# Kernel optimization log

Measured on AMD Instinct MI355X. Metric: run time of the kernel, lower is better.

The kernel has to match this reference:

```python
import jax, jax.numpy as jnp
import numpy as np

D_MODEL = 1024
NUM_HEADS = 16
HEAD_DIM = D_MODEL // NUM_HEADS


def setup_inputs() -> dict:
    key = jax.random.key(0)
    kx, kq, kk, kv, ko = jax.random.split(key, 5)
    B, S = 2, 2048
    scale = 1.0 / np.sqrt(D_MODEL)
    return {
        "x": jax.random.normal(kx, (B, S, D_MODEL), dtype=jnp.float32),
        "W_q": jax.random.normal(kq, (D_MODEL, D_MODEL), dtype=jnp.float32) * scale,
        "W_k": jax.random.normal(kk, (D_MODEL, D_MODEL), dtype=jnp.float32) * scale,
        "W_v": jax.random.normal(kv, (D_MODEL, D_MODEL), dtype=jnp.float32) * scale,
        "W_o": jax.random.normal(ko, (D_MODEL, D_MODEL), dtype=jnp.float32) * scale,
        "causal": 1,
    }


def _attn(x, W_q, W_k, W_v, W_o, causal):
    B, S, D = x.shape
    H, Hd = NUM_HEADS, HEAD_DIM
    # projections: nn.Linear applies x @ W.T
    q = (x @ W_q.T).reshape(B, S, H, Hd)
    k = (x @ W_k.T).reshape(B, S, H, Hd)
    v = (x @ W_v.T).reshape(B, S, H, Hd)
    # scores: [B, H, S, S]
    scores = jnp.einsum("bqhd,bkhd->bhqk", q, k) / np.sqrt(Hd)
    if causal:
        mask = jnp.triu(jnp.ones((S, S), dtype=bool), k=1)
        scores = jnp.where(mask, -jnp.inf, scores)
    attn = jax.nn.softmax(scores, axis=-1)
    out = jnp.einsum("bhqk,bkhd->bqhd", attn, v).reshape(B, S, D)
    return out @ W_o.T


def reference(x, W_q, W_k, W_v, W_o, causal):
    return _attn(x, W_q, W_k, W_v, W_o, causal)
```

## Files before the change

kernel.cpp:

```cpp
#include <hip/hip_runtime.h>

typedef __attribute__((ext_vector_type(8))) short bf16x8;
typedef __attribute__((ext_vector_type(4))) float f32x4;
typedef __attribute__((ext_vector_type(4))) unsigned short u16x4;

#define MFMA16(a, b, c) __builtin_amdgcn_mfma_f32_16x16x32_bf16((a), (b), (c), 0, 0, 0)

static constexpr int D_MODEL = 1024;
static constexpr int SEQ = 2048;
static constexpr int NH = 16;
static constexpr int HD = 64;
static constexpr int LDA = 40;
static constexpr int MST = 136;
static constexpr float NEG_BIG = -1.0e30f;

__device__ __forceinline__ unsigned short f2bf(float f) {
  union { float f; unsigned int u; } v; v.f = f;
  unsigned int r = v.u + 0x7fffu + ((v.u >> 16) & 1u);
  return (unsigned short)(r >> 16);
}

__device__ __forceinline__ unsigned int cvtpk_bf16(float a, float b) {
  unsigned int r;
  asm("v_cvt_pk_bf16_f32 %0, %1, %2" : "=v"(r) : "v"(a), "v"(b));
  return r;
}

__device__ __forceinline__ bf16x8 ld8(const void* p, size_t eidx, int bf) {
  if (bf) return *(const bf16x8*)((const unsigned short*)p + eidx);
  const float* f = (const float*)p + eidx;
  f32x4 lo = *(const f32x4*)f;
  f32x4 hi = *(const f32x4*)(f + 4);
  bf16x8 r;
  r[0] = (short)f2bf(lo[0]); r[1] = (short)f2bf(lo[1]);
  r[2] = (short)f2bf(lo[2]); r[3] = (short)f2bf(lo[3]);
  r[4] = (short)f2bf(hi[0]); r[5] = (short)f2bf(hi[1]);
  r[6] = (short)f2bf(hi[2]); r[7] = (short)f2bf(hi[3]);
  return r;
}

__device__ __forceinline__ void async16(const unsigned short* g, unsigned short* l) {
  __builtin_amdgcn_global_load_lds(
      (const __attribute__((address_space(1))) void*)g,
      (__attribute__((address_space(3))) void*)l, 16, 0, 0);
}

__global__ __launch_bounds__(64) void detect_kernel(
    const unsigned short* __restrict__ xs, int* __restrict__ flag) {
  int lane = threadIdx.x;
  unsigned short s = xs[2 * lane];
  int e = (s >> 7) & 0xFF;
  bool hit = (e >= 117 && e <= 129);
  unsigned long long m = __ballot(hit);
  if (lane == 0) { flag[0] = (__popcll(m) >= 32) ? 1 : 0; flag[1] = 1; }
}

__global__ __launch_bounds__(256) void convert_kernel(
    const void* __restrict__ X,
    const void* __restrict__ W0, const void* __restrict__ W1,
    const void* __restrict__ W2, const void* __restrict__ W3,
    const int* __restrict__ flag,
    unsigned short* __restrict__ Xb, unsigned short* __restrict__ Wb)
{
  const int bf = *flag;
  const int ty = blockIdx.y;
  const void* src; unsigned short* dst; size_t n;
  if (ty == 0) { src = X; dst = Xb; n = (size_t)2 * SEQ * D_MODEL; }
  else {
    src = (ty == 1) ? W0 : (ty == 2) ? W1 : (ty == 3) ? W2 : W3;
    dst = Wb + (size_t)(ty - 1) * D_MODEL * D_MODEL;
    n = (size_t)D_MODEL * D_MODEL;
  }
  size_t i = ((size_t)blockIdx.x * 256 + threadIdx.x) * 8;
  if (i >= n) return;
  *(bf16x8*)(dst + i) = ld8(src, i, bf);
}

__device__ __forceinline__ void gemm_fast_core(
    const unsigned short* __restrict__ A, const unsigned short* __restrict__ B,
    int tm, int tn, unsigned short* smem, f32x4 acc[4][4])
{
  const int t = threadIdx.x;
  const int lane = t & 63;
  const int w = t >> 6;
  const int wm = (w >> 1) * 64, wn = (w & 1) * 64;
  const int quad = lane >> 4, l16 = lane & 15;
  const int srow = lane >> 3;
  const int scol = ((lane & 7) ^ srow) * 8;
  const int xa = l16 & 7;

#pragma unroll
  for (int mi = 0; mi < 4; ++mi)
#pragma unroll
    for (int ni = 0; ni < 4; ++ni)
      acc[mi][ni] = (f32x4){0.f, 0.f, 0.f, 0.f};

#pragma unroll
  for (int j = 0; j < 4; ++j) {
    const int row = w * 32 + j * 8;
    async16(A + (size_t)(tm + row + srow) * D_MODEL + scol, smem + row * 64);
    async16(B + (size_t)(tn + row + srow) * D_MODEL + scol,
            smem + 8192 + row * 64);
  }

  for (int kt = 0; kt < 16; ++kt) {
    const int co = (kt & 1) << 14;
    asm volatile("s_waitcnt vmcnt(0)" ::: "memory");
    __syncthreads();
    if (kt < 15) {
      const int no = ((kt & 1) ^ 1) << 14;
      const int k0 = (kt + 1) * 64;
#pragma unroll
      for (int j = 0; j < 4; ++j) {
        const int row = w * 32 + j * 8;
        async16(A + (size_t)(tm + row + srow) * D_MODEL + k0 + scol,
                smem + no + row * 64);
        async16(B + (size_t)(tn + row + srow) * D_MODEL + k0 + scol,
                smem + no + 8192 + row * 64);
      }
    }
    bf16x8 af[2][4], bfv[2][4];
#pragma unroll
    for (int ks = 0; ks < 2; ++ks) {
#pragma unroll
      for (int mi = 0; mi < 4; ++mi)
        af[ks][mi] = *(const bf16x8*)(smem + co + (wm + mi * 16 + l16) * 64 +
                                      ((ks * 4 + quad) ^ xa) * 8);
#pragma unroll
      for (int ni = 0; ni < 4; ++ni)
        bfv[ks][ni] = *(const bf16x8*)(smem + co + 8192 +
                                       (wn + ni * 16 + l16) * 64 +
                                       ((ks * 4 + quad) ^ xa) * 8);
    }
    __builtin_amdgcn_s_setprio(1);
#pragma unroll
    for (int ks = 0; ks < 2; ++ks)
#pragma unroll
      for (int mi = 0; mi < 4; ++mi)
#pragma unroll
        for (int ni = 0; ni < 4; ++ni)
          acc[mi][ni] = MFMA16(af[ks][mi], bfv[ks][ni], acc[mi][ni]);
    __builtin_amdgcn_s_setprio(0);
  }
}

__global__ __launch_bounds__(256) void qkv_fast_kernel(
    const unsigned short* __restrict__ X,
    const unsigned short* __restrict__ Wb,
    unsigned short* __restrict__ qd,
    unsigned short* __restrict__ kws,
    unsigned short* __restrict__ vws)
{
  __shared__ __align__(16) unsigned short smem[4 * 128 * 64];
  const int bid = blockIdx.x;
  const int xcd = bid & 7, s0 = bid >> 3;
  const int tmg = xcd >> 2, tng = xcd & 3;
  const int tm_local = s0 / 6, zt = s0 % 6;
  const int z = zt >> 1, tn_local = zt & 1;
  const int tm = (tmg * 16 + tm_local) * 128;
  const int tn = (tng * 2 + tn_local) * 128;
  const unsigned short* W = Wb + (size_t)z * D_MODEL * D_MODEL;
  f32x4 acc[4][4];
  gemm_fast_core(X, W, tm, tn, smem, acc);

  const int t = threadIdx.x;
  const int lane = t & 63, w = t >> 6;
  const int wm = (w >> 1) * 64, wn = (w & 1) * 64;
  const int quad = lane >> 4, l16 = lane & 15;

  if (z == 2) {
    const int b = tm >> 11;
    const int sb = tm & 2047;
#pragma unroll
    for (int ph = 0; ph < 2; ++ph) {
      __syncthreads();
      if ((w & 1) == ph) {
#pragma unroll
        for (int mi = 0; mi < 4; ++mi)
#pragma unroll
          for (int ni = 0; ni < 4; ++ni)
#pragma unroll
            for (int r = 0; r < 4; ++r) {
              int m_local = wm + mi * 16 + quad * 4 + r;
              int n_sub = ni * 16 + l16;
              smem[n_sub * MST + m_local] = f2bf(acc[mi][ni][r]);
            }
      }
      __syncthreads();
      const int row = t >> 2, c0 = (t & 3) * 32;
      const int n_g = tn + ph * 64 + row;
      const int h = n_g >> 6, d = n_g & 63;
      unsigned short* dst = vws + (((size_t)b * NH + h) * HD + d) * SEQ + sb + c0;
#pragma unroll
      for (int cc = 0; cc < 4; ++cc)
        *(bf16x8*)(dst + cc * 8) = *(const bf16x8*)(smem + row * MST + c0 + cc * 8);
    }
    return;
  }
#pragma unroll
  for (int mi = 0; mi < 4; ++mi)
#pragma unroll
    for (int ni = 0; ni < 4; ++ni)
#pragma unroll
      for (int r = 0; r < 4; ++r) {
        int m = tm + wm + mi * 16 + quad * 4 + r;
        int n = tn + wn + ni * 16 + l16;
        unsigned short bv = f2bf(acc[mi][ni][r]);
        if (z == 0) {
          qd[(size_t)m * D_MODEL + n] = bv;
        } else {
          int b = m >> 11, sg = m & 2047;
          int h = n >> 6, d = n & 63;
          kws[(((size_t)b * NH + h) * SEQ + sg) * HD + d] = bv;
        }
      }
}

__global__ __launch_bounds__(256) void oproj_fast_kernel(
    const unsigned short* __restrict__ AW,
    const unsigned short* __restrict__ Wo,
    float* __restrict__ tmp)
{
  __shared__ __align__(16) unsigned short smem[4 * 128 * 64];
  const int bid = blockIdx.x;
  const int xcd = bid & 7, s0 = bid >> 3;
  const int tmg = xcd >> 2, tng = xcd & 3;
  const int tm = (tmg * 16 + (s0 >> 1)) * 128;
  const int tn = (tng * 2 + (s0 & 1)) * 128;
  f32x4 acc[4][4];
  gemm_fast_core(AW, Wo, tm, tn, smem, acc);

  const int t = threadIdx.x;
  const int lane = t & 63, w = t >> 6;
  const int wm = (w >> 1) * 64, wn = (w & 1) * 64;
  const int quad = lane >> 4, l16 = lane & 15;
#pragma unroll
  for (int mi = 0; mi < 4; ++mi)
#pragma unroll
    for (int ni = 0; ni < 4; ++ni)
#pragma unroll
      for (int r = 0; r < 4; ++r) {
        int m = tm + wm + mi * 16 + quad * 4 + r;
        int n = tn + wn + ni * 16 + l16;
        tmp[(size_t)m * D_MODEL + n] = acc[mi][ni][r];
      }
}

__device__ __forceinline__ void gemm_tile_128x128(
    const void* __restrict__ A, const void* __restrict__ B, int bf,
    int tm, int tn, unsigned short* As, unsigned short* Bs, f32x4 acc[4][4])
{
  const int t = threadIdx.x;
  const int lane = t & 63;
  const int w = t >> 6;
  const int wm = (w >> 1) * 64, wn = (w & 1) * 64;
  const int quad = lane >> 4, l16 = lane & 15;
  const int r0 = t >> 2, kc = (t & 3) * 8;
  const int r1 = r0 + 64;

#pragma unroll
  for (int mi = 0; mi < 4; ++mi)
#pragma unroll
    for (int ni = 0; ni < 4; ++ni)
      acc[mi][ni] = (f32x4){0.f, 0.f, 0.f, 0.f};

  for (int k0 = 0; k0 < D_MODEL; k0 += 32) {
    bf16x8 a0 = ld8(A, (size_t)(tm + r0) * D_MODEL + k0 + kc, bf);
    bf16x8 a1 = ld8(A, (size_t)(tm + r1) * D_MODEL + k0 + kc, bf);
    bf16x8 b0 = ld8(B, (size_t)(tn + r0) * D_MODEL + k0 + kc, bf);
    bf16x8 b1 = ld8(B, (size_t)(tn + r1) * D_MODEL + k0 + kc, bf);
    __syncthreads();
    *(bf16x8*)(As + r0 * LDA + kc) = a0;
    *(bf16x8*)(As + r1 * LDA + kc) = a1;
    *(bf16x8*)(Bs + r0 * LDA + kc) = b0;
    *(bf16x8*)(Bs + r1 * LDA + kc) = b1;
    __syncthreads();
    bf16x8 af[4], bfv[4];
#pragma unroll
    for (int mi = 0; mi < 4; ++mi)
      af[mi] = *(const bf16x8*)(As + (wm + mi * 16 + l16) * LDA + quad * 8);
#pragma unroll
    for (int ni = 0; ni < 4; ++ni)
      bfv[ni] = *(const bf16x8*)(Bs + (wn + ni * 16 + l16) * LDA + quad * 8);
#pragma unroll
    for (int mi = 0; mi < 4; ++mi)
#pragma unroll
      for (int ni = 0; ni < 4; ++ni)
        acc[mi][ni] = MFMA16(af[mi], bfv[ni], acc[mi][ni]);
  }
}

__global__ __launch_bounds__(256) void qkv_kernel(
    const void* __restrict__ X,
    const void* __restrict__ Wq,
    const void* __restrict__ Wk,
    const void* __restrict__ Wv,
    const int* __restrict__ flag,
    unsigned short* __restrict__ qd,
    unsigned short* __restrict__ kws,
    unsigned short* __restrict__ vws)
{
  __shared__ __align__(16) unsigned short As[128 * LDA];
  __shared__ __align__(16) unsigned short Bs[128 * LDA];
  const int bf = *flag;
  const int z = blockIdx.z;
  const void* W = (z == 0) ? Wq : ((z == 1) ? Wk : Wv);
  const int tm = blockIdx.y * 128, tn = blockIdx.x * 128;
  f32x4 acc[4][4];
  gemm_tile_128x128(X, W, bf, tm, tn, As, Bs, acc);

  const int t = threadIdx.x;
  const int lane = t & 63, w = t >> 6;
  const int wm = (w >> 1) * 64, wn = (w & 1) * 64;
  const int quad = lane >> 4, l16 = lane & 15;
#pragma unroll
  for (int mi = 0; mi < 4; ++mi)
#pragma unroll
    for (int ni = 0; ni < 4; ++ni)
#pragma unroll
      for (int r = 0; r < 4; ++r) {
        int m = tm + wm + mi * 16 + quad * 4 + r;
        int n = tn + wn + ni * 16 + l16;
        unsigned short bv = f2bf(acc[mi][ni][r]);
        if (z == 0) {
          qd[(size_t)m * D_MODEL + n] = bv;
        } else {
          int b = m >> 11, s = m & 2047;
          int h = n >> 6, d = n & 63;
          if (z == 1) kws[(((size_t)b * NH + h) * SEQ + s) * HD + d] = bv;
          else        vws[(((size_t)b * NH + h) * HD + d) * SEQ + s] = bv;
        }
      }
}

__global__ __launch_bounds__(256) void oproj_kernel(
    const unsigned short* __restrict__ AW,
    const void* __restrict__ Wo,
    const int* __restrict__ flag,
    float* __restrict__ tmp)
{
  __shared__ __align__(16) unsigned short As[128 * LDA];
  __shared__ __align__(16) unsigned short Bs[128 * LDA];
  const int bf = *flag;
  const int t = threadIdx.x;
  const int lane = t & 63;
  const int w = t >> 6;
  const int wm = (w >> 1) * 64, wn = (w & 1) * 64;
  const int quad = lane >> 4, l16 = lane & 15;
  const int r0 = t >> 2, kc = (t & 3) * 8;
  const int r1 = r0 + 64;
  const int tm = blockIdx.y * 128, tn = blockIdx.x * 128;
  f32x4 acc[4][4];
#pragma unroll
  for (int mi = 0; mi < 4; ++mi)
#pragma unroll
    for (int ni = 0; ni < 4; ++ni)
      acc[mi][ni] = (f32x4){0.f, 0.f, 0.f, 0.f};

  for (int k0 = 0; k0 < D_MODEL; k0 += 32) {
    bf16x8 a0 = *(const bf16x8*)(AW + (size_t)(tm + r0) * D_MODEL + k0 + kc);
    bf16x8 a1 = *(const bf16x8*)(AW + (size_t)(tm + r1) * D_MODEL + k0 + kc);
    bf16x8 b0 = ld8(Wo, (size_t)(tn + r0) * D_MODEL + k0 + kc, bf);
    bf16x8 b1 = ld8(Wo, (size_t)(tn + r1) * D_MODEL + k0 + kc, bf);
    __syncthreads();
    *(bf16x8*)(As + r0 * LDA + kc) = a0;
    *(bf16x8*)(As + r1 * LDA + kc) = a1;
    *(bf16x8*)(Bs + r0 * LDA + kc) = b0;
    *(bf16x8*)(Bs + r1 * LDA + kc) = b1;
    __syncthreads();
    bf16x8 af[4], bfv[4];
#pragma unroll
    for (int mi = 0; mi < 4; ++mi)
      af[mi] = *(const bf16x8*)(As + (wm + mi * 16 + l16) * LDA + quad * 8);
#pragma unroll
    for (int ni = 0; ni < 4; ++ni)
      bfv[ni] = *(const bf16x8*)(Bs + (wn + ni * 16 + l16) * LDA + quad * 8);
#pragma unroll
    for (int mi = 0; mi < 4; ++mi)
#pragma unroll
      for (int ni = 0; ni < 4; ++ni)
        acc[mi][ni] = MFMA16(af[mi], bfv[ni], acc[mi][ni]);
  }
#pragma unroll
  for (int mi = 0; mi < 4; ++mi)
#pragma unroll
    for (int ni = 0; ni < 4; ++ni)
#pragma unroll
      for (int r = 0; r < 4; ++r) {
        int m = tm + wm + mi * 16 + quad * 4 + r;
        int n = tn + wn + ni * 16 + l16;
        tmp[(size_t)m * D_MODEL + n] = acc[mi][ni][r];
      }
}

__device__ __forceinline__ void attn_item(
    const unsigned short* __restrict__ Ksb, const unsigned short* __restrict__ Vsb,
    const bf16x8 (&aq)[2][2], f32x4 (&oaccT)[2][4], float (&lsum)[2],
    int kt, int diag, int q0base, int l16, int quad, int xa, float Cs)
{
  bf16x8 kfr[4][2], vfr[4][2];
#pragma unroll
  for (int cb = 0; cb < 4; ++cb)
#pragma unroll
    for (int hf = 0; hf < 2; ++hf) {
      kfr[cb][hf] = *(const bf16x8*)(Ksb + (cb * 16 + l16) * 64 +
                                     ((hf * 4 + quad) ^ xa) * 8);
      vfr[cb][hf] = *(const bf16x8*)(Vsb + (cb * 16 + l16) * 64 +
                                     ((hf * 4 + quad) ^ xa) * 8);
    }
#pragma unroll
  for (int s = 0; s < 2; ++s) {
    f32x4 sc[4];
    __builtin_amdgcn_s_setprio(1);
#pragma unroll
    for (int cb = 0; cb < 4; ++cb) {
      sc[cb] = (f32x4){0.f, 0.f, 0.f, 0.f};
      sc[cb] = MFMA16(kfr[cb][0], aq[s][0], sc[cb]);
      sc[cb] = MFMA16(kfr[cb][1], aq[s][1], sc[cb]);
    }
    __builtin_amdgcn_s_setprio(0);
    if (diag) {
      int qq = q0base + s * 16 + l16;
#pragma unroll
      for (int cb = 0; cb < 4; ++cb)
#pragma unroll
        for (int rr = 0; rr < 4; ++rr)
          if (kt * 64 + (cb & 1) * 32 + quad * 8 + (cb >> 1) * 4 + rr > qq)
            sc[cb][rr] = NEG_BIG;
    }
    float ls = 0.f;
#pragma unroll
    for (int cb = 0; cb < 4; ++cb)
#pragma unroll
      for (int rr = 0; rr < 4; ++rr) {
        float pv = __builtin_amdgcn_exp2f(sc[cb][rr] * Cs);
        ls += pv;
        sc[cb][rr] = pv;
      }
    lsum[s] += ls;
    bf16x8 bp[2];
#pragma unroll
    for (int hf = 0; hf < 2; ++hf) {
      union { unsigned int w4[4]; bf16x8 v; } u;
      u.w4[0] = cvtpk_bf16(sc[hf][0], sc[hf][1]);
      u.w4[1] = cvtpk_bf16(sc[hf][2], sc[hf][3]);
      u.w4[2] = cvtpk_bf16(sc[2 + hf][0], sc[2 + hf][1]);
      u.w4[3] = cvtpk_bf16(sc[2 + hf][2], sc[2 + hf][3]);
      bp[hf] = u.v;
    }
    __builtin_amdgcn_s_setprio(1);
#pragma unroll
    for (int db = 0; db < 4; ++db) {
      oaccT[s][db] = MFMA16(vfr[db][0], bp[0], oaccT[s][db]);
      oaccT[s][db] = MFMA16(vfr[db][1], bp[1], oaccT[s][db]);
    }
    __builtin_amdgcn_s_setprio(0);
  }
}

__global__ __launch_bounds__(128, 1) void attn_kernel(
    unsigned short* __restrict__ Qd,
    const unsigned short* __restrict__ Kb,
    const unsigned short* __restrict__ Vt,
    const int* __restrict__ causal_p)
{
  __shared__ __align__(16) unsigned short Ks[3][64 * 64];
  __shared__ __align__(16) unsigned short Vs[3][64 * 64];
  const int bid = blockIdx.x;
  const int xcd = bid & 7, slot = bid >> 3;
  const int bhl = slot >> 4, p = slot & 15;
  const int bh = xcd * 4 + bhl;
  const int b = bh >> 4, h = bh & 15;
  const int t = threadIdx.x, lane = t & 63, w = t >> 6;
  const int quad = lane >> 4, l16 = lane & 15;
  const int causal = *causal_p;
  const int tA = causal ? (31 - p) : (2 * p);
  const int tB = causal ? p : (2 * p + 1);
  const int ktA = causal ? (32 - p) : 32;
  const int ITEMS = causal ? 33 : 64;
  unsigned short* qh = Qd + (size_t)b * SEQ * D_MODEL + h * HD;
  const unsigned short* kh = Kb + ((size_t)b * NH + h) * SEQ * HD;
  const unsigned short* vh = Vt + ((size_t)b * NH + h) * HD * SEQ;
  const float Cs = 0.125f * 1.4426950408889634f;
  const int srow = lane >> 3;
  const int gcol = ((lane & 7) ^ srow) * 8;
  const int xa = l16 & 7;

  int kvp[4];
#pragma unroll
  for (int j2 = 0; j2 < 4; ++j2) {
    const int rp = w * 32 + j2 * 8 + srow;
    kvp[j2] = ((rp >> 4) & 1) * 32 + ((rp >> 2) & 3) * 8 + ((rp >> 5) & 1) * 4 + (rp & 3);
  }

  const int qA = tA * 64 + w * 32, qB = tB * 64 + w * 32;
  bf16x8 aqA[2][2], aqB[2][2];
#pragma unroll
  for (int s = 0; s < 2; ++s)
#pragma unroll
    for (int ch = 0; ch < 2; ++ch) {
      aqA[s][ch] = *(const bf16x8*)(qh + (size_t)(qA + s * 16 + l16) * D_MODEL +
                                    ch * 32 + quad * 8);
      aqB[s][ch] = *(const bf16x8*)(qh + (size_t)(qB + s * 16 + l16) * D_MODEL +
                                    ch * 32 + quad * 8);
    }

  f32x4 oaccA[2][4], oaccB[2][4];
#pragma unroll
  for (int s = 0; s < 2; ++s)
#pragma unroll
    for (int db = 0; db < 4; ++db) {
      oaccA[s][db] = (f32x4){0.f, 0.f, 0.f, 0.f};
      oaccB[s][db] = (f32x4){0.f, 0.f, 0.f, 0.f};
    }
  float lsumA[2] = {0.f, 0.f}, lsumB[2] = {0.f, 0.f};

  auto stage = [&](int f, int buf) {
    const int kt = (f < ktA) ? f : (f - ktA);
#pragma unroll
    for (int j2 = 0; j2 < 4; ++j2) {
      const int row = w * 32 + j2 * 8;
      async16(kh + (size_t)(kt * 64 + kvp[j2]) * HD + gcol, &Ks[buf][row * 64]);
      async16(vh + (size_t)(row + srow) * SEQ + kt * 64 + gcol, &Vs[buf][row * 64]);
    }
  };

  stage(0, 0);
  stage(1, 1);

  int cur = 0, nb = 2;
  for (int f = 0; f < ITEMS; ++f) {
    if (f + 1 < ITEMS) asm volatile("s_waitcnt vmcnt(8)" ::: "memory");
    else               asm volatile("s_waitcnt vmcnt(0)" ::: "memory");
    __builtin_amdgcn_s_barrier();
    __builtin_amdgcn_sched_barrier(0);
    if (f + 2 < ITEMS) stage(f + 2, nb);
    if (f < ktA)
      attn_item(&Ks[cur][0], &Vs[cur][0], aqA, oaccA, lsumA,
                f, causal && (f == ktA - 1), qA, l16, quad, xa, Cs);
    else
      attn_item(&Ks[cur][0], &Vs[cur][0], aqB, oaccB, lsumB,
                f - ktA, causal && (f == ITEMS - 1), qB, l16, quad, xa, Cs);
    cur = (cur == 2) ? 0 : cur + 1;
    nb = (nb == 2) ? 0 : nb + 1;
  }

#pragma unroll
  for (int s = 0; s < 2; ++s) {
    float l = lsumA[s];
    l += __shfl_xor(l, 16, 64);
    l += __shfl_xor(l, 32, 64);
    float inv = 1.0f / l;
#pragma unroll
    for (int db = 0; db < 4; ++db) {
      u16x4 o;
#pragma unroll
      for (int rr = 0; rr < 4; ++rr) o[rr] = f2bf(oaccA[s][db][rr] * inv);
      *(u16x4*)(qh + (size_t)(qA + s * 16 + l16) * D_MODEL + db * 16 + quad * 4) = o;
    }
  }
#pragma unroll
  for (int s = 0; s < 2; ++s) {
    float l = lsumB[s];
    l += __shfl_xor(l, 16, 64);
    l += __shfl_xor(l, 32, 64);
    float inv = 1.0f / l;
#pragma unroll
    for (int db = 0; db < 4; ++db) {
      u16x4 o;
#pragma unroll
      for (int rr = 0; rr < 4; ++rr) o[rr] = f2bf(oaccB[s][db][rr] * inv);
      *(u16x4*)(qh + (size_t)(qB + s * 16 + l16) * D_MODEL + db * 16 + quad * 4) = o;
    }
  }
}

__global__ __launch_bounds__(256) void final_kernel(
    const float* __restrict__ tmp, void* __restrict__ out,
    const int* __restrict__ flag)
{
  const int bf = *flag;
  size_t i = ((size_t)blockIdx.x * 256 + threadIdx.x) * 8;
  f32x4 lo = *(const f32x4*)(tmp + i);
  f32x4 hi = *(const f32x4*)(tmp + i + 4);
  if (bf) {
    bf16x8 r;
    r[0] = (short)f2bf(lo[0]); r[1] = (short)f2bf(lo[1]);
    r[2] = (short)f2bf(lo[2]); r[3] = (short)f2bf(lo[3]);
    r[4] = (short)f2bf(hi[0]); r[5] = (short)f2bf(hi[1]);
    r[6] = (short)f2bf(hi[2]); r[7] = (short)f2bf(hi[3]);
    *(bf16x8*)((unsigned short*)out + i) = r;
  } else {
    *(f32x4*)((float*)out + i) = lo;
    *(f32x4*)((float*)out + i + 4) = hi;
  }
}

extern "C" void kernel_launch(void* const* d_in, const int* in_sizes, int n_in,
                              void* d_out, int out_size, void* d_ws, size_t ws_size,
                              hipStream_t stream) {
  const void* X  = d_in[0];
  const void* Wq = d_in[1];
  const void* Wk = d_in[2];
  const void* Wv = d_in[3];
  const void* Wo = d_in[4];
  const int* causal = (const int*)d_in[5];

  const size_t NE = (size_t)2 * SEQ * D_MODEL;
  const size_t WE = (size_t)D_MODEL * D_MODEL;
  int* flag0 = (int*)d_ws;
  unsigned short* kws = (unsigned short*)((char*)d_ws + 64);
  unsigned short* vws = kws + NE;
  float* tmp = (float*)kws;
  unsigned short* Wb = vws + NE;
  unsigned short* qd = (unsigned short*)d_out;
  unsigned short* Xb = qd + NE;

  const bool big = ws_size >= (size_t)64 + 24ull * 1024 * 1024;

  hipLaunchKernelGGL(detect_kernel, dim3(1), dim3(64), 0, stream,
                     (const unsigned short*)X, flag0);
  if (big) {
    hipLaunchKernelGGL(convert_kernel, dim3(2048, 5), dim3(256), 0, stream,
                       X, Wq, Wk, Wv, Wo, flag0, Xb, Wb);
    hipLaunchKernelGGL(qkv_fast_kernel, dim3(768), dim3(256), 0, stream,
                       Xb, Wb, qd, kws, vws);
    hipLaunchKernelGGL(attn_kernel, dim3(512), dim3(128), 0, stream,
                       qd, kws, vws, causal);
    hipLaunchKernelGGL(oproj_fast_kernel, dim3(256), dim3(256), 0, stream,
                       qd, Wb + 3 * WE, tmp);
  } else {
    hipLaunchKernelGGL(qkv_kernel, dim3(8, 32, 3), dim3(256), 0, stream,
                       X, Wq, Wk, Wv, flag0, qd, kws, vws);
    hipLaunchKernelGGL(attn_kernel, dim3(512), dim3(128), 0, stream,
                       qd, kws, vws, causal);
    hipLaunchKernelGGL(oproj_kernel, dim3(8, 32), dim3(256), 0, stream,
                       qd, Wo, flag0, tmp);
  }
  hipLaunchKernelGGL(final_kernel, dim3(2048), dim3(256), 0, stream,
                     tmp, d_out, flag0);
}
```

Measured before the change: 200.1 us.

## Switch projection GEMM core to triple-buffered BK=32 pipeline with partial waits

The shared GEMM core used by the QKV and output projections moves from double-buffered 64-wide K tiles to triple-buffered 32-wide K tiles. It waits only for the oldest outstanding loads (vmcnt(4)) instead of draining all of them, and it uses a raw barrier. The swizzle is adapted to the 32-column layout, and LDS per block shrinks from 64KB to 48KB, which may allow more resident blocks. The aim is to hide global load latency better. In exchange it issues twice as many barriers and K iterations, each with less MFMA work.

```diff
diff --git a/kernel.cpp b/kernel.cpp
--- a/kernel.cpp
+++ b/kernel.cpp
@@ -85,9 +85,9 @@
   const int w = t >> 6;
   const int wm = (w >> 1) * 64, wn = (w & 1) * 64;
   const int quad = lane >> 4, l16 = lane & 15;
-  const int srow = lane >> 3;
-  const int scol = ((lane & 7) ^ srow) * 8;
-  const int xa = l16 & 7;
+  const int srow = lane >> 2;
+  const int scol = ((lane & 3) ^ ((lane >> 3) & 3)) * 8;
+  const int xa = (l16 >> 1) & 3;
 
 #pragma unroll
   for (int mi = 0; mi < 4; ++mi)
@@ -95,52 +95,47 @@
     for (int ni = 0; ni < 4; ++ni)
       acc[mi][ni] = (f32x4){0.f, 0.f, 0.f, 0.f};
 
-#pragma unroll
-  for (int j = 0; j < 4; ++j) {
-    const int row = w * 32 + j * 8;
-    async16(A + (size_t)(tm + row + srow) * D_MODEL + scol, smem + row * 64);
-    async16(B + (size_t)(tn + row + srow) * D_MODEL + scol,
-            smem + 8192 + row * 64);
-  }
-
-  for (int kt = 0; kt < 16; ++kt) {
-    const int co = (kt & 1) << 14;
-    asm volatile("s_waitcnt vmcnt(0)" ::: "memory");
-    __syncthreads();
-    if (kt < 15) {
-      const int no = ((kt & 1) ^ 1) << 14;
-      const int k0 = (kt + 1) * 64;
-#pragma unroll
-      for (int j = 0; j < 4; ++j) {
-        const int row = w * 32 + j * 8;
-        async16(A + (size_t)(tm + row + srow) * D_MODEL + k0 + scol,
-                smem + no + row * 64);
-        async16(B + (size_t)(tn + row + srow) * D_MODEL + k0 + scol,
-                smem + no + 8192 + row * 64);
-      }
-    }
-    bf16x8 af[2][4], bfv[2][4];
-#pragma unroll
-    for (int ks = 0; ks < 2; ++ks) {
-#pragma unroll
-      for (int mi = 0; mi < 4; ++mi)
-        af[ks][mi] = *(const bf16x8*)(smem + co + (wm + mi * 16 + l16) * 64 +
-                                      ((ks * 4 + quad) ^ xa) * 8);
+  auto stage = [&](int f, int buf) {
+    const int k0 = f * 32;
+    unsigned short* dst = smem + buf * 8192;
+#pragma unroll
+    for (int i = 0; i < 2; ++i) {
+      const int row = w * 32 + i * 16;
+      async16(A + (size_t)(tm + row + srow) * D_MODEL + k0 + scol,
+              dst + row * 32);
+      async16(B + (size_t)(tn + row + srow) * D_MODEL + k0 + scol,
+              dst + 4096 + row * 32);
+    }
+  };
+
+  stage(0, 0);
+  stage(1, 1);
+
+  int cur = 0, nb = 2;
+  for (int f = 0; f < 32; ++f) {
+    if (f + 1 < 32) asm volatile("s_waitcnt vmcnt(4)" ::: "memory");
+    else            asm volatile("s_waitcnt vmcnt(0)" ::: "memory");
+    __builtin_amdgcn_s_barrier();
+    __builtin_amdgcn_sched_barrier(0);
+    if (f + 2 < 32) stage(f + 2, nb);
+    const unsigned short* As = smem + cur * 8192;
+    const unsigned short* Bs = As + 4096;
+    bf16x8 af[4], bfv[4];
+#pragma unroll
+    for (int mi = 0; mi < 4; ++mi)
+      af[mi] = *(const bf16x8*)(As + (wm + mi * 16 + l16) * 32 + (quad ^ xa) * 8);
+#pragma unroll
+    for (int ni = 0; ni < 4; ++ni)
+      bfv[ni] = *(const bf16x8*)(Bs + (wn + ni * 16 + l16) * 32 + (quad ^ xa) * 8);
+    __builtin_amdgcn_s_setprio(1);
+#pragma unroll
+    for (int mi = 0; mi < 4; ++mi)
 #pragma unroll
       for (int ni = 0; ni < 4; ++ni)
-        bfv[ks][ni] = *(const bf16x8*)(smem + co + 8192 +
-                                       (wn + ni * 16 + l16) * 64 +
-                                       ((ks * 4 + quad) ^ xa) * 8);
-    }
-    __builtin_amdgcn_s_setprio(1);
-#pragma unroll
-    for (int ks = 0; ks < 2; ++ks)
-#pragma unroll
-      for (int mi = 0; mi < 4; ++mi)
-#pragma unroll
-        for (int ni = 0; ni < 4; ++ni)
-          acc[mi][ni] = MFMA16(af[ks][mi], bfv[ks][ni], acc[mi][ni]);
+        acc[mi][ni] = MFMA16(af[mi], bfv[ni], acc[mi][ni]);
     __builtin_amdgcn_s_setprio(0);
+    cur = (cur == 2) ? 0 : cur + 1;
+    nb = (nb == 2) ? 0 : nb + 1;
   }
 }
 
@@ -151,7 +146,7 @@
     unsigned short* __restrict__ kws,
     unsigned short* __restrict__ vws)
 {
-  __shared__ __align__(16) unsigned short smem[4 * 128 * 64];
+  __shared__ __align__(16) unsigned short smem[3 * 8192];
   const int bid = blockIdx.x;
   const int xcd = bid & 7, s0 = bid >> 3;
   const int tmg = xcd >> 2, tng = xcd & 3;
@@ -221,7 +216,7 @@
     const unsigned short* __restrict__ Wo,
     float* __restrict__ tmp)
 {
-  __shared__ __align__(16) unsigned short smem[4 * 128 * 64];
+  __shared__ __align__(16) unsigned short smem[3 * 8192];
   const int bid = blockIdx.x;
   const int xcd = bid & 7, s0 = bid >> 3;
   const int tmg = xcd >> 2, tng = xcd & 3;
```

Measured after the change: 194.6 us. 2.8% less time.
